# Kernel tuning notes

Measured on AMD Instinct MI355X. Metric: run time of the kernel, lower is better.

Reference implementation:

```python
import jax, jax.numpy as jnp
import numpy as np

LANE_WEIGHT = 1.0   # _LANE_LOSS_WEIGHT
TEMP = 0.1          # args.score_temp

B, L, K, T = 256, 16, 64, 50
NL, NT = B * L, B * L * K


def _seg_ids(starts, n):
    # contiguous segments covering [0, n): segment id = (# starts <= i) - 1
    return (jnp.cumsum(jnp.zeros((n,), jnp.int32).at[starts].add(1)) - 1).astype(jnp.int32)


def _seg_log_softmax(x, seg, nseg):
    m = jax.ops.segment_max(x, seg, num_segments=nseg)
    z = x - m[seg]
    lse = jnp.log(jax.ops.segment_sum(jnp.exp(z), seg, num_segments=nseg))
    return z - lse[seg]


def _seg_softmax(x, seg, nseg):
    m = jax.ops.segment_max(x, seg, num_segments=nseg)
    e = jnp.exp(x - m[seg])
    s = jax.ops.segment_sum(e, seg, num_segments=nseg)
    return e / s[seg]


def setup_inputs() -> dict:
    key = jax.random.key(0)
    k1, k2, k3, k4, k5 = jax.random.split(key, 5)
    lane_scores = jax.random.normal(k1, (NL,), jnp.float32)
    traj_scores = jax.random.normal(k2, (NT, 1), jnp.float32)
    pred_candidates = jax.random.normal(k3, (NT, T, 2), jnp.float32)
    pred_gt = jax.random.normal(k4, (B, T, 2), jnp.float32)
    scales = jnp.ones((B,), jnp.float32)
    # ragged segment boundaries (here uniform, but reference only uses starts)
    cls_start_end_idx = jnp.stack([jnp.arange(B, dtype=jnp.int32) * L,
                                   jnp.arange(B, dtype=jnp.int32) * L + L], axis=1)
    trajs_start_end_idx = jnp.stack([jnp.arange(NL, dtype=jnp.int32) * K,
                                     jnp.arange(NL, dtype=jnp.int32) * K + K], axis=1)
    cls_oracle = jax.random.bernoulli(k5, 0.3, (NL,))
    # guarantee >= 1 oracle lane per sample (original divides by len(traj_loss))
    cls_oracle = cls_oracle.at[jnp.arange(B) * L].set(True)
    return {
        "lane_scores": lane_scores,
        "traj_scores": traj_scores,
        "pred_candidates": pred_candidates,
        "pred_gt": pred_gt,
        "scales": scales,
        "cls_oracle": cls_oracle,
        "cls_start_end_idx": cls_start_end_idx,
        "trajs_start_end_idx": trajs_start_end_idx,
    }


def reference(lane_scores, traj_scores, pred_candidates, pred_gt, scales,
              cls_oracle, cls_start_end_idx, trajs_start_end_idx):
    nl, nt = lane_scores.shape[0], traj_scores.shape[0]
    b = cls_start_end_idx.shape[0]
    lane_sample = _seg_ids(cls_start_end_idx[:, 0], nl)   # [NL] -> sample id
    traj_lane = _seg_ids(trajs_start_end_idx[:, 0], nt)   # [NT] -> lane id
    traj_sample = lane_sample[traj_lane]                  # [NT] -> sample id

    # ---- lane-level cross entropy per sample ----
    oracle_f = cls_oracle.astype(lane_scores.dtype)
    oracle_per_sample = jax.ops.segment_sum(oracle_f, lane_sample, num_segments=b)
    lane_target = oracle_f / oracle_per_sample[lane_sample]
    lane_logp = _seg_log_softmax(lane_scores, lane_sample, b)
    lane_loss = jax.ops.segment_sum(-lane_target * lane_logp, lane_sample,
                                    num_segments=b) * LANE_WEIGHT  # [B]

    # ---- trajectory-level cross entropy per oracle lane ----
    # ScoreEvaluator.scoring_trajs: ADE distance to GT, scale-normalized, negated
    diff = pred_candidates - pred_gt[traj_sample]          # [NT, T, 2]
    ade = jnp.mean(jnp.sqrt(jnp.sum(diff * diff, axis=-1) + 1e-12), axis=-1)
    scores = -ade / scales[traj_sample]                    # [NT]

    target = _seg_softmax(scores / TEMP, traj_lane, nl)    # softmax(scores/temp)
    out_logp = _seg_log_softmax(traj_scores[:, 0], traj_lane, nl)
    ce_per_lane = jax.ops.segment_sum(-target * out_logp, traj_lane,
                                      num_segments=nl)     # [NL]
    # only oracle lanes contribute; average over oracle-lane count per sample
    traj_loss = jax.ops.segment_sum(ce_per_lane * oracle_f, lane_sample,
                                    num_segments=b) / oracle_per_sample  # [B]

    return jnp.mean(lane_loss + traj_loss)
```

## Files before the change

### kernel.cpp

```cpp
#include <hip/hip_runtime.h>
#include <math.h>


#define LANE_WEIGHT 1.0f
#define TEMP_INV    10.0f

typedef float v4f __attribute__((ext_vector_type(4)));

__global__ __launch_bounds__(1024) void dual_classify_sample(
    const float* __restrict__ pred_candidates,
    const float* __restrict__ pred_gt,
    const float* __restrict__ traj_scores,
    const float* __restrict__ scales,
    const float* __restrict__ lane_scores,
    const int*   __restrict__ cls_oracle,
    const int*   __restrict__ cls_se,
    const int*   __restrict__ trajs_se,
    float*       __restrict__ out,
    int B, int T)
{
    const int sample = blockIdx.x;
    const int wid    = threadIdx.x >> 6;
    const int lid    = threadIdx.x & 63;
    const int nwaves = blockDim.x >> 6;

    const int cs   = cls_se[2 * sample];
    const int cend = cls_se[2 * sample + 1];
    const int nl   = cend - cs;

    __shared__ float s_ce[64];

    const int nf4 = (T * 2) / 4;
    const v4f* __restrict__ gp =
        (const v4f*)(pred_gt + (size_t)sample * (T * 2));
    const float inv_scale = 1.0f / scales[sample];

    for (int li = wid; li < nl; li += nwaves) {
        const int lane = cs + li;
        const int t0 = trajs_se[2 * lane];
        const int Kl = trajs_se[2 * lane + 1] - t0;

        const bool valid = (lid < Kl);
        const int  traj  = t0 + (valid ? lid : (Kl > 0 ? Kl - 1 : 0));
        const v4f* __restrict__ tp =
            (const v4f*)(pred_candidates + (size_t)traj * (T * 2));

        float sum = 0.0f;
        #pragma unroll 5
        for (int r = 0; r < nf4; ++r) {
            v4f c = tp[r];
            v4f g = gp[r];
            float dx0 = c.x - g.x, dy0 = c.y - g.y;
            float dx1 = c.z - g.z, dy1 = c.w - g.w;
            sum += sqrtf(dx0 * dx0 + dy0 * dy0 + 1e-12f)
                 + sqrtf(dx1 * dx1 + dy1 * dy1 + 1e-12f);
        }
        if ((T & 1) != 0) {
            const float2* tp2 = (const float2*)tp;
            const float2* gp2 = (const float2*)gp;
            float2 c = tp2[2 * nf4], g = gp2[2 * nf4];
            float dx = c.x - g.x, dy = c.y - g.y;
            sum += sqrtf(dx * dx + dy * dy + 1e-12f);
        }

        float sc = valid ? (-(sum / (float)T) * inv_scale * TEMP_INV)
                         : -INFINITY;
        float m = sc;
        for (int off = 32; off; off >>= 1) m = fmaxf(m, __shfl_xor(m, off));
        float e = valid ? expf(sc - m) : 0.0f;
        float Z = e;
        for (int off = 32; off; off >>= 1) Z += __shfl_xor(Z, off);
        float target = e / Z;

        float tsc = valid ? traj_scores[traj] : -INFINITY;
        float m2 = tsc;
        for (int off = 32; off; off >>= 1) m2 = fmaxf(m2, __shfl_xor(m2, off));
        float e2 = valid ? expf(tsc - m2) : 0.0f;
        float Z2 = e2;
        for (int off = 32; off; off >>= 1) Z2 += __shfl_xor(Z2, off);
        float logp = (tsc - m2) - logf(Z2);

        float ce = valid ? (-target * logp) : 0.0f;
        for (int off = 32; off; off >>= 1) ce += __shfl_xor(ce, off);
        if (lid == 0) s_ce[li] = ce;
    }
    __syncthreads();

    if (wid == 0) {
        const bool v = (lid < nl);
        const int  l = cs + (v ? lid : 0);

        float sc = v ? lane_scores[l] : -INFINITY;
        float m = sc;
        for (int off = 32; off; off >>= 1) m = fmaxf(m, __shfl_xor(m, off));
        float e = v ? expf(sc - m) : 0.0f;
        float Z = e;
        for (int off = 32; off; off >>= 1) Z += __shfl_xor(Z, off);
        const float lse = m + logf(Z);

        const bool o = v && (cls_oracle[l] != 0);
        float cnt = o ? 1.0f : 0.0f;
        float ll  = o ? -(sc - lse) : 0.0f;
        float tl  = o ? s_ce[lid]   : 0.0f;
        for (int off = 32; off; off >>= 1) {
            cnt += __shfl_xor(cnt, off);
            ll  += __shfl_xor(ll,  off);
            tl  += __shfl_xor(tl,  off);
        }
        if (lid == 0) {
            const float sample_loss =
                (ll * LANE_WEIGHT + tl) / cnt;
            atomicAdd(out, sample_loss / (float)B);
        }
    }
}

extern "C" void kernel_launch(void* const* d_in, const int* in_sizes, int n_in,
                              void* d_out, int out_size, void* d_ws, size_t ws_size,
                              hipStream_t stream)
{
    const float* lane_scores     = (const float*)d_in[0];
    const float* traj_scores     = (const float*)d_in[1];
    const float* pred_candidates = (const float*)d_in[2];
    const float* pred_gt         = (const float*)d_in[3];
    const float* scales          = (const float*)d_in[4];
    const int*   cls_oracle      = (const int*)d_in[5];
    const int*   cls_se          = (const int*)d_in[6];
    const int*   trajs_se        = (const int*)d_in[7];

    const int NT = in_sizes[1];
    const int B  = in_sizes[6] / 2;
    const int T  = in_sizes[2] / (NT * 2);

    float* out = (float*)d_out;

    dual_classify_sample<<<B, 1024, 0, stream>>>(
        pred_candidates, pred_gt, traj_scores, scales, lane_scores,
        cls_oracle, cls_se, trajs_se, out, B, T);
}
```

Before: 177.8 us.

## Stage trajectory candidates into LDS with coalesced global_load_lds for T=50

Adds a specialized kernel for T=50 that copies each lane's contiguous trajectory block into shared memory using global_load_lds 16-byte transfers, so global reads are fully coalesced instead of strided per-thread reads. It also caches the ground truth in LDS and cuts the block to 4 waves so more blocks can be resident per CU. The trade-offs are about 100KB of LDS per block, which limits occupancy, an explicit vmcnt wait that stops load/compute overlap, and LDS bank conflicts from the stride-25 float4 reads.

```diff
diff --git a/kernel.cpp b/kernel.cpp
--- a/kernel.cpp
+++ b/kernel.cpp
@@ -5,7 +5,130 @@
 #define LANE_WEIGHT 1.0f
 #define TEMP_INV    10.0f
 
+#define TT     50
+#define FPT    25
+#define NWAVES 4
+
 typedef float v4f __attribute__((ext_vector_type(4)));
+
+typedef __attribute__((address_space(1))) const unsigned int gu32;
+typedef __attribute__((address_space(3))) unsigned int       lu32;
+
+__device__ __forceinline__ void stage16(const float* g, v4f* l)
+{
+    __builtin_amdgcn_global_load_lds((gu32*)g, (lu32*)l, 16, 0, 0);
+}
+
+__global__ __launch_bounds__(256) void dual_classify_fast(
+    const float* __restrict__ pred_candidates,
+    const float* __restrict__ pred_gt,
+    const float* __restrict__ traj_scores,
+    const float* __restrict__ scales,
+    const float* __restrict__ lane_scores,
+    const int*   __restrict__ cls_oracle,
+    const int*   __restrict__ cls_se,
+    const int*   __restrict__ trajs_se,
+    float*       __restrict__ out,
+    int B)
+{
+    __shared__ v4f   buf[NWAVES][64 * FPT];
+    __shared__ v4f   s_gt[FPT];
+    __shared__ float s_ce[64];
+
+    const int sample = blockIdx.x;
+    const int wid    = threadIdx.x >> 6;
+    const int lid    = threadIdx.x & 63;
+
+    const int cs = cls_se[2 * sample];
+    const int nl = cls_se[2 * sample + 1] - cs;
+
+    if (threadIdx.x < FPT)
+        s_gt[threadIdx.x] =
+            ((const v4f*)(pred_gt + (size_t)sample * (2 * TT)))[threadIdx.x];
+    const float inv_scale = 1.0f / scales[sample];
+    __syncthreads();
+
+    for (int li = wid; li < nl; li += NWAVES) {
+        const int lane = cs + li;
+        const int t0   = trajs_se[2 * lane];
+        const int Kl   = trajs_se[2 * lane + 1] - t0;
+        const int NF   = Kl * FPT;
+
+        const float* gbase  = pred_candidates + (size_t)t0 * (2 * TT);
+        const int    ncalls = (NF + 63) >> 6;
+        for (int r = 0; r < ncalls; ++r) {
+            const int idx = (r << 6) + lid;
+            if (idx < NF)
+                stage16(gbase + (size_t)idx * 4, &buf[wid][r << 6]);
+        }
+        asm volatile("s_waitcnt vmcnt(0)" ::: "memory");
+
+        const bool valid = (lid < Kl);
+        float sum = 0.0f;
+        {
+            const v4f* tp = &buf[wid][lid * FPT];
+            #pragma unroll 5
+            for (int j = 0; j < FPT; ++j) {
+                v4f c = tp[j];
+                v4f g = s_gt[j];
+                float dx0 = c.x - g.x, dy0 = c.y - g.y;
+                float dx1 = c.z - g.z, dy1 = c.w - g.w;
+                sum += sqrtf(dx0 * dx0 + dy0 * dy0 + 1e-12f)
+                     + sqrtf(dx1 * dx1 + dy1 * dy1 + 1e-12f);
+            }
+        }
+
+        float sc = valid ? (-(sum / (float)TT) * inv_scale * TEMP_INV)
+                         : -INFINITY;
+        float m = sc;
+        for (int off = 32; off; off >>= 1) m = fmaxf(m, __shfl_xor(m, off));
+        float e = valid ? expf(sc - m) : 0.0f;
+        float Z = e;
+        for (int off = 32; off; off >>= 1) Z += __shfl_xor(Z, off);
+        float target = e / Z;
+
+        const int traj = t0 + (valid ? lid : (Kl > 0 ? Kl - 1 : 0));
+        float tsc = valid ? traj_scores[traj] : -INFINITY;
+        float m2 = tsc;
+        for (int off = 32; off; off >>= 1) m2 = fmaxf(m2, __shfl_xor(m2, off));
+        float e2 = valid ? expf(tsc - m2) : 0.0f;
+        float Z2 = e2;
+        for (int off = 32; off; off >>= 1) Z2 += __shfl_xor(Z2, off);
+        float logp = (tsc - m2) - logf(Z2);
+
+        float ce = valid ? (-target * logp) : 0.0f;
+        for (int off = 32; off; off >>= 1) ce += __shfl_xor(ce, off);
+        if (lid == 0) s_ce[li] = ce;
+    }
+    __syncthreads();
+
+    if (wid == 0) {
+        const bool v = (lid < nl);
+        const int  l = cs + (v ? lid : 0);
+
+        float sc = v ? lane_scores[l] : -INFINITY;
+        float m = sc;
+        for (int off = 32; off; off >>= 1) m = fmaxf(m, __shfl_xor(m, off));
+        float e = v ? expf(sc - m) : 0.0f;
+        float Z = e;
+        for (int off = 32; off; off >>= 1) Z += __shfl_xor(Z, off);
+        const float lse = m + logf(Z);
+
+        const bool o = v && (cls_oracle[l] != 0);
+        float cnt = o ? 1.0f : 0.0f;
+        float ll  = o ? -(sc - lse) : 0.0f;
+        float tl  = o ? s_ce[lid]   : 0.0f;
+        for (int off = 32; off; off >>= 1) {
+            cnt += __shfl_xor(cnt, off);
+            ll  += __shfl_xor(ll,  off);
+            tl  += __shfl_xor(tl,  off);
+        }
+        if (lid == 0) {
+            const float sample_loss = (ll * LANE_WEIGHT + tl) / cnt;
+            atomicAdd(out, sample_loss / (float)B);
+        }
+    }
+}
 
 __global__ __launch_bounds__(1024) void dual_classify_sample(
     const float* __restrict__ pred_candidates,
@@ -108,8 +231,7 @@
             tl  += __shfl_xor(tl,  off);
         }
         if (lid == 0) {
-            const float sample_loss =
-                (ll * LANE_WEIGHT + tl) / cnt;
+            const float sample_loss = (ll * LANE_WEIGHT + tl) / cnt;
             atomicAdd(out, sample_loss / (float)B);
         }
     }
@@ -134,7 +256,13 @@
 
     float* out = (float*)d_out;
 
-    dual_classify_sample<<<B, 1024, 0, stream>>>(
-        pred_candidates, pred_gt, traj_scores, scales, lane_scores,
-        cls_oracle, cls_se, trajs_se, out, B, T);
-}
+    if (T == TT) {
+        dual_classify_fast<<<B, NWAVES * 64, 0, stream>>>(
+            pred_candidates, pred_gt, traj_scores, scales, lane_scores,
+            cls_oracle, cls_se, trajs_se, out, B);
+    } else {
+        dual_classify_sample<<<B, 1024, 0, stream>>>(
+            pred_candidates, pred_gt, traj_scores, scales, lane_scores,
+            cls_oracle, cls_se, trajs_se, out, B, T);
+    }
+}
```

Measured after the change: 180.0 us. No clear change (+1.2%).
